# Performance work log

Hardware: AMD Instinct MI355X
Metric: run time of the kernel (lower is better)

## Reference

```python
import jax, jax.numpy as jnp
import numpy as np

NH = 16  # num_heads


def _ln(x, eps=1e-6):
    m = x.mean(-1, keepdims=True)
    v = ((x - m) ** 2).mean(-1, keepdims=True)
    return (x - m) * jax.lax.rsqrt(v + eps)


def _mod(z, sh, sc):
    return z * (1 + sc[:, None, :]) + sh[:, None, :]


def _attn(q, k, v, out_w, out_b, nh=NH):
    B, S, E = q.shape
    hd = E // nh
    q = q.reshape(B, S, nh, hd)
    k = k.reshape(B, -1, nh, hd)
    v = v.reshape(B, -1, nh, hd)
    s = jnp.einsum('bqhd,bkhd->bhqk', q, k) / float(np.sqrt(hd))
    a = jax.nn.softmax(s, axis=-1)
    o = jnp.einsum('bhqk,bkhd->bqhd', a, v).reshape(B, S, E)
    return o @ out_w.T + out_b


def setup_inputs() -> dict:
    key = jax.random.key(0)
    ks = jax.random.split(key, 40)
    E, L, Ne, I, p, C, clip, Kd = 1024, 2, 8, 4096, 2, 4, 768, 1536
    N = (64 // p) ** 2
    n = lambda k, shape, s=0.02: (jax.random.normal(k, shape, jnp.float32) * s)
    inp = {
        'x': jax.random.normal(ks[0], (2, C, 64, 64), jnp.float32),
        't': jax.random.uniform(ks[1], (2,), jnp.float32) * 1000.0,
        'clip_vec': jax.random.normal(ks[2], (2, clip), jnp.float32),
        'qwen_context': jax.random.normal(ks[3], (2, 256, Kd), jnp.float32),
        'conv_w': n(ks[4], (E, C, p, p)),
        'conv_b': n(ks[5], (E,)),
        'pos_embed': n(ks[6], (1, N, E)),
        'tmlp_w1': n(ks[7], (256, 256)), 'tmlp_b1': n(ks[8], (256,)),
        'tmlp_w2': n(ks[9], (256, 256)), 'tmlp_b2': n(ks[10], (256,)),
        'cond_w': n(ks[11], (E, 256 + clip)), 'cond_b': n(ks[12], (E,)),
        'ada_w': n(ks[13], (L, 9 * E, E)), 'ada_b': n(ks[14], (L, 9 * E)),
        'sa_in_w': n(ks[15], (L, 3 * E, E)), 'sa_in_b': n(ks[16], (L, 3 * E)),
        'sa_out_w': n(ks[17], (L, E, E)), 'sa_out_b': n(ks[18], (L, E)),
        'ca_q_w': n(ks[19], (L, E, E)), 'ca_k_w': n(ks[20], (L, E, Kd)),
        'ca_v_w': n(ks[21], (L, E, Kd)), 'ca_in_b': n(ks[22], (L, 3 * E)),
        'ca_out_w': n(ks[23], (L, E, E)), 'ca_out_b': n(ks[24], (L, E)),
        'gate_w': n(ks[25], (L, Ne, E)), 'gate_b': n(ks[26], (L, Ne)),
        'e_w1': n(ks[27], (L, Ne, I, E)), 'e_b1': n(ks[28], (L, Ne, I)),
        'e_w2': n(ks[29], (L, Ne, E, I)), 'e_b2': n(ks[30], (L, Ne, E)),
        'fin_w': n(ks[31], (p * p * C, E)), 'fin_b': n(ks[32], (p * p * C,)),
    }
    return inp


def reference(x, t, clip_vec, qwen_context, conv_w, conv_b, pos_embed,
              tmlp_w1, tmlp_b1, tmlp_w2, tmlp_b2, cond_w, cond_b,
              ada_w, ada_b, sa_in_w, sa_in_b, sa_out_w, sa_out_b,
              ca_q_w, ca_k_w, ca_v_w, ca_in_b, ca_out_w, ca_out_b,
              gate_w, gate_b, e_w1, e_b1, e_w2, e_b2, fin_w, fin_b):
    B, C, H, W = x.shape
    E, p = conv_w.shape[0], conv_w.shape[-1]
    h, w = H // p, W // p
    # patch-embed conv (kernel==stride) as unfold + matmul
    patches = x.reshape(B, C, h, p, w, p).transpose(0, 2, 4, 1, 3, 5).reshape(B, h * w, C * p * p)
    xt = patches @ conv_w.reshape(E, -1).T + conv_b + pos_embed
    # sinusoidal timestep embedding (dim 256)
    half = 128
    freqs = jnp.exp(jnp.arange(half, dtype=jnp.float32) * (-np.log(10000.0) / (half - 1)))
    te = t[:, None] * freqs[None, :]
    te = jnp.concatenate([jnp.sin(te), jnp.cos(te)], -1)
    te = jax.nn.silu(te @ tmlp_w1.T + tmlp_b1) @ tmlp_w2.T + tmlp_b2
    c = jnp.concatenate([te, clip_vec], -1) @ cond_w.T + cond_b  # [B,E]
    depth = ada_w.shape[0]
    for i in range(depth):
        pr = jax.nn.silu(c) @ ada_w[i].T + ada_b[i]
        sh_sa, sc_sa, g_sa, sh_ca, sc_ca, g_ca, sh_m, sc_m, g_m = jnp.split(pr, 9, axis=1)
        # self-attention
        xn = _mod(_ln(xt), sh_sa, sc_sa)
        qkv = xn @ sa_in_w[i].T + sa_in_b[i]
        q, k, v = jnp.split(qkv, 3, axis=-1)
        xt = xt + g_sa[:, None, :] * _attn(q, k, v, sa_out_w[i], sa_out_b[i])
        # cross-attention with separate q/k/v projections
        xn = _mod(_ln(xt), sh_ca, sc_ca)
        q = xn @ ca_q_w[i].T + ca_in_b[i, :E]
        k = qwen_context @ ca_k_w[i].T + ca_in_b[i, E:2 * E]
        v = qwen_context @ ca_v_w[i].T + ca_in_b[i, 2 * E:]
        xt = xt + g_ca[:, None, :] * _attn(q, k, v, ca_out_w[i], ca_out_b[i])
        # top-2 sparse MoE (dense-combine formulation: zero weight for unrouted experts)
        xn = _mod(_ln(xt), sh_m, sc_m)
        probs = jax.nn.softmax(xn @ gate_w[i].T + gate_b[i], axis=-1)
        tw, ti = jax.lax.top_k(probs, 2)
        tw = tw / (tw.sum(-1, keepdims=True) + 1e-6)
        wd = (jax.nn.one_hot(ti, probs.shape[-1], dtype=xn.dtype) * tw[..., None]).sum(-2)  # [B,S,Ne]
        hid = jax.nn.gelu(jnp.einsum('bsd,eid->bsei', xn, e_w1[i]) + e_b1[i], approximate=True)
        y = jnp.einsum('bsei,eoi->bseo', hid, e_w2[i]) + e_b2[i]
        moe = jnp.einsum('bseo,bse->bso', y, wd)
        xt = xt + g_m[:, None, :] * moe
    # final layer + unpatchify (nhwpqc->nchpwq)
    xt = _ln(xt) @ fin_w.T + fin_b
    out = xt.reshape(B, h, w, p, p, C).transpose(0, 5, 1, 3, 2, 4).reshape(B, C, h * p, w * p)
    return out
```

## Files before the change

kernel.cpp:

```cpp
#include <hip/hip_runtime.h>
#include <hip/hip_bf16.h>

#define B_ 2
#define S_ 1024
#define E_ 1024
#define NHEAD 16
#define NE 8
#define II 4096
#define KD 1536
#define CLIP_ 768
#define TOK (B_*S_)
#define NSLOTP 5120

typedef short bf16x8 __attribute__((ext_vector_type(8)));
typedef float f32x4 __attribute__((ext_vector_type(4)));

__device__ __forceinline__ float siluf(float x){ return x/(1.f+expf(-x)); }
__device__ __forceinline__ float geluf(float x){
    float x3 = x*x*x;
    return 0.5f*x*(1.f+tanhf(0.7978845608028654f*(x+0.044715f*x3)));
}
__device__ __forceinline__ unsigned short h16(float x){
    union { __hip_bfloat16 b; unsigned short u; } c;
    c.b = __float2bfloat16(x);
    return c.u;
}
__device__ __forceinline__ unsigned pk2(float a, float b){
    return (unsigned)h16(a) | ((unsigned)h16(b)<<16);
}
__device__ __forceinline__ void sp(float a, unsigned& hb, unsigned& lb){
    unsigned short h = h16(a);
    float r = a - __uint_as_float(((unsigned)h)<<16);
    hb = h; lb = h16(r);
}
__device__ __forceinline__ size_t pidx(int row, int k, int K){
    return (((size_t)(row>>4)*(K>>5) + (k>>5))<<9) + (((k>>3)&3)<<7) + ((row&15)<<3) + (k&7);
}

union U8 { unsigned u[4]; bf16x8 v; uint4 q; };

__global__ void k_patch_embed(const float* __restrict__ x, const float* __restrict__ cw,
                              const float* __restrict__ cb, const float* __restrict__ pos,
                              float* __restrict__ xt){
    int token = blockIdx.x;
    int b = token >> 10, n = token & 1023;
    int hh = n >> 5, ww = n & 31;
    __shared__ float patch[16];
    int tid = threadIdx.x;
    if (tid < 16){
        int c = tid >> 2, py = (tid >> 1) & 1, px = tid & 1;
        patch[tid] = x[(((size_t)b*4 + c)*64 + hh*2+py)*64 + ww*2+px];
    }
    __syncthreads();
    for (int e = tid; e < E_; e += 256){
        float acc = cb[e];
        #pragma unroll
        for (int j=0;j<16;j++) acc += patch[j]*cw[e*16+j];
        xt[(size_t)token*E_ + e] = acc + pos[(size_t)n*E_ + e];
    }
}

__global__ void k_time_cond(const float* __restrict__ t, const float* __restrict__ clip,
                            const float* __restrict__ w1, const float* __restrict__ b1,
                            const float* __restrict__ w2, const float* __restrict__ b2,
                            const float* __restrict__ cw, const float* __restrict__ cbias,
                            float* __restrict__ silu_c){
    int b = blockIdx.x, tid = threadIdx.x;
    __shared__ float te[256], h1[256], te2[256];
    if (tid < 128){
        float f = expf((float)tid * (-9.210340371976184f/127.f));
        float a = t[b]*f;
        te[tid]     = sinf(a);
        te[tid+128] = cosf(a);
    }
    __syncthreads();
    {
        float acc = b1[tid];
        const float* wr = w1 + (size_t)tid*256;
        for (int k=0;k<256;k++) acc += te[k]*wr[k];
        h1[tid] = siluf(acc);
    }
    __syncthreads();
    {
        float acc = b2[tid];
        const float* wr = w2 + (size_t)tid*256;
        for (int k=0;k<256;k++) acc += h1[k]*wr[k];
        te2[tid] = acc;
    }
    __syncthreads();
    const float* cl = clip + (size_t)b*CLIP_;
    for (int e = tid; e < E_; e += 256){
        float acc = cbias[e];
        const float* wr = cw + (size_t)e*1024;
        for (int k=0;k<256;k++)  acc += te2[k]*wr[k];
        for (int k=0;k<CLIP_;k++) acc += cl[k]*wr[256+k];
        silu_c[b*E_+e] = siluf(acc);
    }
}

__global__ void k_ada2(const float* __restrict__ sic, const float* __restrict__ aw,
                       const float* __restrict__ ab, float* __restrict__ pr){
    int row = blockIdx.x*4 + (threadIdx.x>>6);
    int lane = threadIdx.x & 63;
    const float* w = aw + (size_t)row*1024;
    float a0 = 0.f, a1 = 0.f;
    #pragma unroll
    for (int it=0; it<4; it++){
        int k = it*256 + lane*4;
        float4 wv = *(const float4*)(w+k);
        float4 x0 = *(const float4*)(sic+k);
        float4 x1 = *(const float4*)(sic+1024+k);
        a0 += wv.x*x0.x + wv.y*x0.y + wv.z*x0.z + wv.w*x0.w;
        a1 += wv.x*x1.x + wv.y*x1.y + wv.z*x1.z + wv.w*x1.w;
    }
    #pragma unroll
    for (int off=32; off; off>>=1){ a0 += __shfl_down(a0,off); a1 += __shfl_down(a1,off); }
    if (lane==0){
        float bb = ab[row];
        pr[row] = a0 + bb;
        pr[9*E_ + row] = a1 + bb;
    }
}

template<int PACK>
__global__ void k_ln_mod(const float* __restrict__ src, float* __restrict__ dst32,
                         unsigned short* __restrict__ dsth, unsigned short* __restrict__ dstl,
                         const float* __restrict__ pr, int shc, int scc){
    int token = blockIdx.x, tid = threadIdx.x;
    int b = token >> 10;
    const float* row = src + (size_t)token*E_;
    float4 v = *(const float4*)(row + tid*4);
    float s = v.x+v.y+v.z+v.w;
    float ss = v.x*v.x+v.y*v.y+v.z*v.z+v.w*v.w;
    #pragma unroll
    for (int off=32; off; off>>=1){ s += __shfl_down(s,off); ss += __shfl_down(ss,off); }
    __shared__ float rs_[4], rss_[4];
    int wid = tid >> 6;
    if ((tid&63)==0){ rs_[wid]=s; rss_[wid]=ss; }
    __syncthreads();
    s  = rs_[0]+rs_[1]+rs_[2]+rs_[3];
    ss = rss_[0]+rss_[1]+rss_[2]+rss_[3];
    float mean = s*(1.f/1024.f);
    float rstd = rsqrtf(ss*(1.f/1024.f) - mean*mean + 1e-6f);
    const float* shv = pr + b*9*E_ + shc*E_;
    const float* scv = pr + b*9*E_ + scc*E_;
    int e = tid*4;
    float o[4];
    float4 sc4 = *(const float4*)(scv+e);
    float4 sh4 = *(const float4*)(shv+e);
    o[0] = (v.x-mean)*rstd*(1.f+sc4.x) + sh4.x;
    o[1] = (v.y-mean)*rstd*(1.f+sc4.y) + sh4.y;
    o[2] = (v.z-mean)*rstd*(1.f+sc4.z) + sh4.z;
    o[3] = (v.w-mean)*rstd*(1.f+sc4.w) + sh4.w;
    unsigned hu[2], lu[2];
    {
        unsigned h0,l0,h1,l1;
        sp(o[0],h0,l0); sp(o[1],h1,l1);
        hu[0]=h0|(h1<<16); lu[0]=l0|(l1<<16);
        sp(o[2],h0,l0); sp(o[3],h1,l1);
        hu[1]=h0|(h1<<16); lu[1]=l0|(l1<<16);
    }
    if (PACK){
        size_t base = pidx(token, e, E_);
        *(uint2*)(dsth + base) = make_uint2(hu[0],hu[1]);
        *(uint2*)(dstl + base) = make_uint2(lu[0],lu[1]);
    } else {
        *(float4*)(dst32 + (size_t)token*E_ + e) = make_float4(o[0],o[1],o[2],o[3]);
        *(uint2*)(dsth + (size_t)token*E_ + e) = make_uint2(hu[0],hu[1]);
        *(uint2*)(dstl + (size_t)token*E_ + e) = make_uint2(lu[0],lu[1]);
    }
}

__global__ void k_pack_qwen(const float* __restrict__ q, unsigned short* __restrict__ hp,
                            unsigned short* __restrict__ lp){
    int r = blockIdx.x;
    int k = threadIdx.x*8;
    float f[8];
    *(float4*)(f+0) = *(const float4*)(q + (size_t)r*KD + k);
    *(float4*)(f+4) = *(const float4*)(q + (size_t)r*KD + k + 4);
    U8 H, L;
    #pragma unroll
    for (int i=0;i<4;i++){
        unsigned h0,l0,h1,l1;
        sp(f[2*i],h0,l0); sp(f[2*i+1],h1,l1);
        H.u[i] = h0|(h1<<16); L.u[i] = l0|(l1<<16);
    }
    size_t dst = pidx(r, k, KD);
    *(uint4*)(hp + dst) = H.q;
    *(uint4*)(lp + dst) = L.q;
}

__global__ void k_gather_pack(const unsigned short* __restrict__ xh,
                              const unsigned short* __restrict__ xl,
                              const int* __restrict__ list,
                              unsigned short* __restrict__ oh, unsigned short* __restrict__ ol){
    int s = blockIdx.x;
    int tid = threadIdx.x;
    int token = list[s];
    int k = tid*8;
    size_t src = (size_t)token*E_ + k;
    size_t dst = pidx(s, k, E_);
    *(uint4*)(oh + dst) = *(const uint4*)(xh + src);
    *(uint4*)(ol + dst) = *(const uint4*)(xl + src);
}

template<int MOE, int EPI, int TERMS, int SPLITK=1>
__global__ __launch_bounds__(256) void k_mm(
    const unsigned short* __restrict__ Ah, const unsigned short* __restrict__ Al,
    const float* __restrict__ Wp, int ldw,
    const float* __restrict__ biasp, int bstride,
    void* __restrict__ Cp, void* __restrict__ Cp2, int ldc,
    int M, int N, int K,
    const float* __restrict__ pr, int gch,
    const int* __restrict__ cnt, const int* __restrict__ offs)
{
    constexpr int NPL = (TERMS==3) ? 2 : 1;
    int e  = MOE ? blockIdx.z : 0;
    int Mm = MOE ? cnt[e] : M;
    int bm = blockIdx.y*128;
    if (MOE && bm >= Mm) return;
    int o0 = MOE ? offs[e] : 0;
    int nt = gridDim.x / SPLITK;
    int ntile = blockIdx.x % nt;
    int kc = blockIdx.x / nt;
    int bn = ntile*128;
    int kbeg = kc*(K/SPLITK), kend = kbeg + K/SPLITK;
    const float* W = Wp + (size_t)e*N*ldw;
    const float* bias = biasp + (size_t)e*bstride;

    __shared__ __align__(16) unsigned short Bs_[2][NPL][128*40];

    int tid = threadIdx.x;
    int lane = tid & 63, wid = tid >> 6;
    int wm = wid >> 1, wn = wid & 1;
    int fr = lane & 15, fko = (lane>>4)*8, fr4 = (lane>>4)*4;
    int lane8 = lane<<3;
    int K32 = K>>5;

    int rgm[4];
    #pragma unroll
    for (int m=0;m<4;m++) rgm[m] = ((MOE?o0:0) + bm + wm*64 + m*16) >> 4;

    auto LA = [&](int m, int k0, bf16x8& h, bf16x8& l){
        size_t off = (((size_t)rgm[m]*K32 + (k0>>5))<<9) + lane8;
        h = *(const bf16x8*)(Ah + off);
        if (TERMS==3) l = *(const bf16x8*)(Al + off);
    };

    int srow = tid >> 1, shalf = tid & 1;
    int sbase = srow*40 + shalf*16;
    const float* Bf = W + (size_t)(bn + srow)*ldw + shalf*16;

    float fB[16];
    auto LOADB = [&](int k0){
        *(float4*)(fB+0)  = *(const float4*)(Bf+k0+0);
        *(float4*)(fB+4)  = *(const float4*)(Bf+k0+4);
        *(float4*)(fB+8)  = *(const float4*)(Bf+k0+8);
        *(float4*)(fB+12) = *(const float4*)(Bf+k0+12);
    };
    auto STAGEB = [&](int buf){
        if (TERMS==3){
            unsigned hb2[8], lb2[8];
            #pragma unroll
            for (int i=0;i<8;i++){
                unsigned h0,l0,h1,l1;
                sp(fB[2*i],h0,l0); sp(fB[2*i+1],h1,l1);
                hb2[i]=h0|(h1<<16); lb2[i]=l0|(l1<<16);
            }
            *(uint4*)&Bs_[buf][0][sbase]   = make_uint4(hb2[0],hb2[1],hb2[2],hb2[3]);
            *(uint4*)&Bs_[buf][0][sbase+8] = make_uint4(hb2[4],hb2[5],hb2[6],hb2[7]);
            *(uint4*)&Bs_[buf][NPL-1][sbase]   = make_uint4(lb2[0],lb2[1],lb2[2],lb2[3]);
            *(uint4*)&Bs_[buf][NPL-1][sbase+8] = make_uint4(lb2[4],lb2[5],lb2[6],lb2[7]);
        } else {
            unsigned hb2[8];
            #pragma unroll
            for (int i=0;i<8;i++) hb2[i] = pk2(fB[2*i],fB[2*i+1]);
            *(uint4*)&Bs_[buf][0][sbase]   = make_uint4(hb2[0],hb2[1],hb2[2],hb2[3]);
            *(uint4*)&Bs_[buf][0][sbase+8] = make_uint4(hb2[4],hb2[5],hb2[6],hb2[7]);
        }
    };

    f32x4 acc[4][4];
    #pragma unroll
    for (int m=0;m<4;m++)
        #pragma unroll
        for (int n=0;n<4;n++) acc[m][n] = (f32x4){0.f,0.f,0.f,0.f};

    bf16x8 ah[4], al[4];
    #pragma unroll
    for (int m=0;m<4;m++) LA(m, kbeg, ah[m], al[m]);
    LOADB(kbeg);
    STAGEB(0);
    __syncthreads();
    int cur = 0;
    for (int k0=kbeg; k0<kend; k0+=32){
        bool nxt = (k0+32) < kend;
        if (nxt) LOADB(k0+32);
        bf16x8 bh[4], bl[4];
        #pragma unroll
        for (int n=0;n<4;n++){
            int off = (wn*64 + n*16 + fr)*40 + fko;
            bh[n] = *(const bf16x8*)&Bs_[cur][0][off];
            if (TERMS==3) bl[n] = *(const bf16x8*)&Bs_[cur][NPL-1][off];
        }
        #pragma unroll
        for (int m=0;m<4;m++){
            #pragma unroll
            for (int n=0;n<4;n++){
                acc[m][n] = __builtin_amdgcn_mfma_f32_16x16x32_bf16(ah[m], bh[n], acc[m][n], 0, 0, 0);
                if (TERMS==3){
                    acc[m][n] = __builtin_amdgcn_mfma_f32_16x16x32_bf16(ah[m], bl[n], acc[m][n], 0, 0, 0);
                    acc[m][n] = __builtin_amdgcn_mfma_f32_16x16x32_bf16(al[m], bh[n], acc[m][n], 0, 0, 0);
                }
            }
            if (nxt) LA(m, k0+32, ah[m], al[m]);
        }
        if (nxt) STAGEB(cur^1);
        __syncthreads();
        cur ^= 1;
    }

    #pragma unroll
    for (int m=0;m<4;m++){
        #pragma unroll
        for (int j=0;j<4;j++){
            int row = bm + wm*64 + m*16 + fr4 + j;
            if (EPI != 2 && row >= Mm) continue;
            #pragma unroll
            for (int n=0;n<4;n++){
                int col = bn + wn*64 + n*16 + fr;
                float bv = (SPLITK==1 || kc==0) ? bias[col] : 0.f;
                float v = acc[m][n][j] + bv;
                if (EPI==0){
                    ((float*)Cp)[(size_t)row*ldc + col] = v;
                } else if (EPI==1){
                    int bb = row >> 10;
                    ((float*)Cp)[(size_t)row*ldc + col] += pr[bb*9*E_ + gch*E_ + col] * v;
                } else if (EPI==2){
                    int prow = o0 + row;
                    size_t pi = pidx(prow, col, II);
                    if (TERMS==3){
                        unsigned hb, lb; sp(geluf(v), hb, lb);
                        ((unsigned short*)Cp )[pi] = (unsigned short)hb;
                        ((unsigned short*)Cp2)[pi] = (unsigned short)lb;
                    } else {
                        ((unsigned short*)Cp )[pi] = h16(geluf(v));
                    }
                } else {
                    if (SPLITK==1)
                        ((float*)Cp)[(size_t)(o0+row)*ldc + col] = v;
                    else
                        atomicAdd(&((float*)Cp)[(size_t)(o0+row)*ldc + col], v);
                }
            }
        }
    }
}

__global__ __launch_bounds__(256) void k_attn_m(
    const float* __restrict__ qp, int qstride,
    const float* __restrict__ kp, const float* __restrict__ vp, int kvstride,
    unsigned short* __restrict__ oph, unsigned short* __restrict__ opl,
    int Sq, int Sk, float scale)
{
    __shared__ __align__(16) unsigned short Kh[64*72];
    __shared__ __align__(16) unsigned short Kl[64*72];
    __shared__ __align__(16) unsigned V_i[64*70];
    __shared__ __align__(16) unsigned short P_[4][2][16*72];

    int tid = threadIdx.x, lane = tid & 63, wid = tid >> 6;
    int g = lane >> 4, fr = lane & 15;
    int h = blockIdx.y, b = blockIdx.z;
    int qbase = blockIdx.x*64;

    bf16x8 qh[2], ql[2];
    {
        const float* qr = qp + (size_t)(b*Sq + qbase + wid*16 + fr)*qstride + h*64;
        #pragma unroll
        for (int ds=0; ds<2; ds++){
            float f[8];
            *(float4*)(f+0) = *(const float4*)(qr + ds*32 + g*8);
            *(float4*)(f+4) = *(const float4*)(qr + ds*32 + g*8 + 4);
            U8 uh, ul;
            #pragma unroll
            for (int i=0;i<4;i++){
                unsigned h0,l0,h1,l1;
                sp(f[2*i]*scale, h0,l0); sp(f[2*i+1]*scale, h1,l1);
                uh.u[i] = h0|(h1<<16); ul.u[i] = l0|(l1<<16);
            }
            qh[ds] = uh.v; ql[ds] = ul.v;
        }
    }

    float m_run = -1e30f, l_run = 0.f;
    f32x4 oacc[4];
    #pragma unroll
    for (int dt=0;dt<4;dt++) oacc[dt] = (f32x4){0.f,0.f,0.f,0.f};

    unsigned short* PhW = &P_[wid][0][0];
    unsigned short* PlW = &P_[wid][1][0];

    for (int kt0 = 0; kt0 < Sk; kt0 += 64){
        __syncthreads();
        {
            int srow = tid >> 2, d0 = (tid & 3) << 4;
            size_t grow = (size_t)(b*Sk + kt0 + srow)*kvstride + h*64 + d0;
            {
                const float* srcp = kp + grow;
                float f[16];
                *(float4*)(f+0)  = *(const float4*)(srcp+0);
                *(float4*)(f+4)  = *(const float4*)(srcp+4);
                *(float4*)(f+8)  = *(const float4*)(srcp+8);
                *(float4*)(f+12) = *(const float4*)(srcp+12);
                U8 uh0, uh1, ul0, ul1;
                #pragma unroll
                for (int i=0;i<4;i++){
                    unsigned a0,b0,a1,b1;
                    sp(f[2*i],a0,b0); sp(f[2*i+1],a1,b1);
                    uh0.u[i] = a0|(a1<<16); ul0.u[i] = b0|(b1<<16);
                }
                #pragma unroll
                for (int i=0;i<4;i++){
                    unsigned a0,b0,a1,b1;
                    sp(f[8+2*i],a0,b0); sp(f[8+2*i+1],a1,b1);
                    uh1.u[i] = a0|(a1<<16); ul1.u[i] = b0|(b1<<16);
                }
                int base = srow*72 + d0;
                *(uint4*)&Kh[base]     = uh0.q;
                *(uint4*)&Kh[base + 8] = uh1.q;
                *(uint4*)&Kl[base]     = ul0.q;
                *(uint4*)&Kl[base + 8] = ul1.q;
            }
            {
                const float* srcp = vp + grow;
                float f[16];
                *(float4*)(f+0)  = *(const float4*)(srcp+0);
                *(float4*)(f+4)  = *(const float4*)(srcp+4);
                *(float4*)(f+8)  = *(const float4*)(srcp+8);
                *(float4*)(f+12) = *(const float4*)(srcp+12);
                int base = srow*70 + d0;
                #pragma unroll
                for (int i4=0;i4<4;i4++){
                    U8 u;
                    #pragma unroll
                    for (int i=0;i<4;i++){
                        unsigned hb, lb; sp(f[4*i4+i], hb, lb);
                        u.u[i] = hb | (lb<<16);
                    }
                    *(uint2*)&V_i[base + i4*4]     = make_uint2(u.u[0], u.u[1]);
                    *(uint2*)&V_i[base + i4*4 + 2] = make_uint2(u.u[2], u.u[3]);
                }
            }
        }
        __syncthreads();

        f32x4 st[4];
        #pragma unroll
        for (int kt=0;kt<4;kt++) st[kt] = (f32x4){0.f,0.f,0.f,0.f};
        #pragma unroll
        for (int ds=0; ds<2; ds++){
            #pragma unroll
            for (int kt=0;kt<4;kt++){
                int row = kt*16 + fr;
                int so = row*72 + ds*32 + g*8;
                bf16x8 kh  = *(const bf16x8*)&Kh[so];
                bf16x8 klo = *(const bf16x8*)&Kl[so];
                st[kt] = __builtin_amdgcn_mfma_f32_16x16x32_bf16(kh, qh[ds], st[kt], 0,0,0);
                st[kt] = __builtin_amdgcn_mfma_f32_16x16x32_bf16(kh, ql[ds], st[kt], 0,0,0);
                st[kt] = __builtin_amdgcn_mfma_f32_16x16x32_bf16(klo, qh[ds], st[kt], 0,0,0);
            }
        }

        float pmax = -1e30f;
        #pragma unroll
        for (int kt=0;kt<4;kt++)
            #pragma unroll
            for (int r=0;r<4;r++) pmax = fmaxf(pmax, st[kt][r]);
        pmax = fmaxf(pmax, __shfl_xor(pmax, 16));
        pmax = fmaxf(pmax, __shfl_xor(pmax, 32));
        float mnew = fmaxf(m_run, pmax);
        float p[4][4]; float psum = 0.f;
        #pragma unroll
        for (int kt=0;kt<4;kt++)
            #pragma unroll
            for (int r=0;r<4;r++){ float pv = expf(st[kt][r] - mnew); p[kt][r] = pv; psum += pv; }
        psum += __shfl_xor(psum, 16);
        psum += __shfl_xor(psum, 32);
        float corr = expf(m_run - mnew);
        l_run = l_run*corr + psum;
        m_run = mnew;
        #pragma unroll
        for (int j=0;j<4;j++){
            float cj = __shfl(corr, g*4 + j);
            #pragma unroll
            for (int dt=0;dt<4;dt++) oacc[dt][j] *= cj;
        }

        #pragma unroll
        for (int kt=0;kt<4;kt++){
            unsigned h0,l0,h1,l1,h2,l2,h3,l3;
            sp(p[kt][0],h0,l0); sp(p[kt][1],h1,l1);
            sp(p[kt][2],h2,l2); sp(p[kt][3],h3,l3);
            int base = fr*72 + kt*16 + g*4;
            *(unsigned*)&PhW[base]     = h0|(h1<<16);
            *(unsigned*)&PhW[base + 2] = h2|(h3<<16);
            *(unsigned*)&PlW[base]     = l0|(l1<<16);
            *(unsigned*)&PlW[base + 2] = l2|(l3<<16);
        }

        #pragma unroll
        for (int ks=0; ks<2; ks++){
            int pso = fr*72 + ks*32 + g*8;
            bf16x8 ph = *(const bf16x8*)&PhW[pso];
            bf16x8 pl = *(const bf16x8*)&PlW[pso];
            #pragma unroll
            for (int dt=0; dt<4; dt++){
                unsigned w[8];
                #pragma unroll
                for (int j=0;j<8;j++){
                    int row = ks*32 + g*8 + j;
                    w[j] = V_i[row*70 + dt*16 + fr];
                }
                U8 vh, vl;
                #pragma unroll
                for (int i=0;i<4;i++){
                    vh.u[i] = (w[2*i] & 0xffffu) | (w[2*i+1] << 16);
                    vl.u[i] = (w[2*i] >> 16)     | (w[2*i+1] & 0xffff0000u);
                }
                oacc[dt] = __builtin_amdgcn_mfma_f32_16x16x32_bf16(ph, vh.v, oacc[dt], 0,0,0);
                oacc[dt] = __builtin_amdgcn_mfma_f32_16x16x32_bf16(ph, vl.v, oacc[dt], 0,0,0);
                oacc[dt] = __builtin_amdgcn_mfma_f32_16x16x32_bf16(pl, vh.v, oacc[dt], 0,0,0);
            }
        }
    }

    float linv = 1.f / l_run;
    #pragma unroll
    for (int j=0;j<4;j++){
        float lj = __shfl(linv, g*4 + j);
        int row = b*Sq + qbase + wid*16 + g*4 + j;
        #pragma unroll
        for (int dt=0;dt<4;dt++){
            unsigned hb, lb; sp(oacc[dt][j]*lj, hb, lb);
            int k = h*64 + dt*16 + fr;
            size_t pi = pidx(row, k, E_);
            oph[pi] = (unsigned short)hb;
            opl[pi] = (unsigned short)lb;
        }
    }
}

__global__ void k_route(const float* __restrict__ xn, const float* __restrict__ gw,
                        const float* __restrict__ gb, int* __restrict__ i01,
                        float* __restrict__ w01, int* __restrict__ cnt){
    int token = blockIdx.x, lane = threadIdx.x;
    const float* row = xn + (size_t)token*E_;
    float part[8] = {0,0,0,0,0,0,0,0};
    for (int k = lane; k < E_; k += 64){
        float xv = row[k];
        #pragma unroll
        for (int e=0;e<8;e++) part[e] += xv*gw[e*E_+k];
    }
    #pragma unroll
    for (int e=0;e<8;e++){
        #pragma unroll
        for (int off=32; off; off>>=1) part[e] += __shfl_down(part[e], off);
    }
    if (lane==0){
        float lg[8]; float mx = -1e30f;
        #pragma unroll
        for (int e=0;e<8;e++){ lg[e] = part[e]+gb[e]; if (lg[e]>mx) mx = lg[e]; }
        float sum = 0.f;
        #pragma unroll
        for (int e=0;e<8;e++){ lg[e] = expf(lg[e]-mx); sum += lg[e]; }
        int a0 = 0;
        #pragma unroll
        for (int e=1;e<8;e++) if (lg[e] > lg[a0]) a0 = e;
        int a1 = (a0==0)?1:0;
        #pragma unroll
        for (int e=0;e<8;e++) if (e!=a0 && lg[e] > lg[a1]) a1 = e;
        float p0 = lg[a0]/sum, p1 = lg[a1]/sum;
        float inv = 1.f/(p0+p1+1e-6f);
        i01[token*2+0]=a0; i01[token*2+1]=a1;
        w01[token*2+0]=p0*inv; w01[token*2+1]=p1*inv;
        atomicAdd(&cnt[a0],1); atomicAdd(&cnt[a1],1);
    }
}

__global__ void k_scan(const int* __restrict__ cnt, int* __restrict__ offs, int* __restrict__ curs){
    if (threadIdx.x==0 && blockIdx.x==0){
        int o = 0;
        for (int e=0;e<8;e++){
            offs[e]=o; curs[e]=o;
            o += ((cnt[e]+127)>>7)<<7;
        }
    }
}

__global__ void k_place(const int* __restrict__ i01,
                        int* __restrict__ curs, int* __restrict__ list,
                        int* __restrict__ t2s){
    int t = blockIdx.x*256 + threadIdx.x;
    if (t >= TOK) return;
    #pragma unroll
    for (int s=0;s<2;s++){
        int e = i01[t*2+s];
        int p = atomicAdd(&curs[e],1);
        list[p] = t;
        t2s[t*2+s] = p;
    }
}

__global__ void k_moe_combine2(float* __restrict__ xt, const float* __restrict__ yslot,
                               const int* __restrict__ t2s, const float* __restrict__ w01,
                               const float* __restrict__ pr){
    int idx = blockIdx.x*256 + threadIdx.x;
    int token = idx >> 10, n = idx & 1023;
    int b = token >> 10;
    int s0 = t2s[token*2], s1 = t2s[token*2+1];
    float mo = w01[token*2]*yslot[(size_t)s0*E_+n] + w01[token*2+1]*yslot[(size_t)s1*E_+n];
    xt[idx] += pr[b*9*E_ + 8*E_ + n]*mo;
}

__global__ void k_final(const float* __restrict__ xt, const float* __restrict__ fw,
                        const float* __restrict__ fb, float* __restrict__ out){
    int token = blockIdx.x, tid = threadIdx.x;
    int b = token >> 10, n = token & 1023, hh = n >> 5, ww = n & 31;
    const float* row = xt + (size_t)token*E_;
    float4 v = *(const float4*)(row + tid*4);
    float s = v.x+v.y+v.z+v.w;
    float ss = v.x*v.x+v.y*v.y+v.z*v.z+v.w*v.w;
    #pragma unroll
    for (int off=32; off; off>>=1){ s += __shfl_down(s,off); ss += __shfl_down(ss,off); }
    __shared__ float rs_[4], rss_[4];
    int wid = tid >> 6;
    if ((tid&63)==0){ rs_[wid]=s; rss_[wid]=ss; }
    __syncthreads();
    s  = rs_[0]+rs_[1]+rs_[2]+rs_[3];
    ss = rss_[0]+rss_[1]+rss_[2]+rss_[3];
    float mean = s*(1.f/1024.f);
    float rstd = rsqrtf(ss*(1.f/1024.f) - mean*mean + 1e-6f);
    __shared__ float xl[1024];
    int e = tid*4;
    xl[e+0]=(v.x-mean)*rstd; xl[e+1]=(v.y-mean)*rstd;
    xl[e+2]=(v.z-mean)*rstd; xl[e+3]=(v.w-mean)*rstd;
    __syncthreads();
    int o = tid & 15, seg = tid >> 4;
    float part = 0.f;
    const float* wr = fw + (size_t)o*E_ + seg*64;
    const float* xr = xl + seg*64;
    #pragma unroll 8
    for (int j=0;j<64;j++) part += xr[j]*wr[j];
    __shared__ float ps[16][17];
    ps[seg][o] = part;
    __syncthreads();
    if (tid < 16){
        float acc = fb[tid];
        #pragma unroll
        for (int s2=0;s2<16;s2++) acc += ps[s2][tid];
        int py = tid>>3, px = (tid>>2)&1, ch = tid&3;
        out[(((size_t)b*4+ch)*64 + hh*2+py)*64 + ww*2+px] = acc;
    }
}

extern "C" void kernel_launch(void* const* d_in, const int* in_sizes, int n_in,
                              void* d_out, int out_size, void* d_ws, size_t ws_size,
                              hipStream_t stream){
    const float* x        = (const float*)d_in[0];
    const float* t        = (const float*)d_in[1];
    const float* clip     = (const float*)d_in[2];
    const float* qwen     = (const float*)d_in[3];
    const float* conv_w   = (const float*)d_in[4];
    const float* conv_b   = (const float*)d_in[5];
    const float* pos      = (const float*)d_in[6];
    const float* tw1      = (const float*)d_in[7];
    const float* tb1      = (const float*)d_in[8];
    const float* tw2      = (const float*)d_in[9];
    const float* tb2      = (const float*)d_in[10];
    const float* cond_w   = (const float*)d_in[11];
    const float* cond_b   = (const float*)d_in[12];
    const float* ada_w    = (const float*)d_in[13];
    const float* ada_b    = (const float*)d_in[14];
    const float* sa_in_w  = (const float*)d_in[15];
    const float* sa_in_b  = (const float*)d_in[16];
    const float* sa_out_w = (const float*)d_in[17];
    const float* sa_out_b = (const float*)d_in[18];
    const float* ca_q_w   = (const float*)d_in[19];
    const float* ca_k_w   = (const float*)d_in[20];
    const float* ca_v_w   = (const float*)d_in[21];
    const float* ca_in_b  = (const float*)d_in[22];
    const float* ca_out_w = (const float*)d_in[23];
    const float* ca_out_b = (const float*)d_in[24];
    const float* gate_w   = (const float*)d_in[25];
    const float* gate_b   = (const float*)d_in[26];
    const float* e_w1     = (const float*)d_in[27];
    const float* e_b1     = (const float*)d_in[28];
    const float* e_w2     = (const float*)d_in[29];
    const float* e_b2     = (const float*)d_in[30];
    const float* fin_w    = (const float*)d_in[31];
    const float* fin_b    = (const float*)d_in[32];

    float* ws    = (float*)d_ws;
    float* xt    = ws;
    float* xn    = ws + 2097152;
    float* qkv   = ws + 4194304;
    float* yslot = qkv;
    unsigned short* xnh  = (unsigned short*)(ws + 10485760);
    unsigned short* xnl  = (unsigned short*)(ws + 11534336);
    unsigned short* obh  = (unsigned short*)(ws + 12582912);
    unsigned short* obl  = (unsigned short*)(ws + 13631488);
    unsigned short* xnsh = (unsigned short*)(ws + 14680064);
    unsigned short* xnsl = (unsigned short*)(ws + 17301504);
    unsigned short* hidh = (unsigned short*)(ws + 19922944);
    unsigned short* hidl = (unsigned short*)(ws + 30408704);
    unsigned short* qwph = (unsigned short*)(ws + 40894464);
    unsigned short* qwpl = (unsigned short*)(ws + 41287680);
    float* kbuf  = ws + 41680896;
    float* vbuf  = ws + 42205184;
    float* pr    = ws + 42729472;
    float* sic   = ws + 42747904;
    float* w01   = ws + 42749952;
    int*   i01   = (int*)(ws + 42754048);
    int*   t2s   = (int*)(ws + 42758144);
    int*   list  = (int*)(ws + 42762240);
    int*   cnt   = (int*)(ws + 42767360);
    int*   offs  = cnt + 8;
    int*   curs  = cnt + 16;

    k_patch_embed<<<TOK,256,0,stream>>>(x, conv_w, conv_b, pos, xt);
    k_time_cond<<<B_,256,0,stream>>>(t, clip, tw1, tb1, tw2, tb2, cond_w, cond_b, sic);
    k_pack_qwen<<<B_*256,192,0,stream>>>(qwen, qwph, qwpl);

    for (int i=0;i<2;i++){
        k_ada2<<<2304,256,0,stream>>>(sic, ada_w + (size_t)i*9*E_*E_,
                                      ada_b + (size_t)i*9*E_, pr);
        k_ln_mod<1><<<TOK,256,0,stream>>>(xt, nullptr, xnh, xnl, pr, 0, 1);
        k_mm<0,0,3><<<dim3(24,16),256,0,stream>>>(
            xnh, xnl, sa_in_w + (size_t)i*3*E_*E_, E_, sa_in_b + (size_t)i*3*E_, 0,
            qkv, nullptr, 3*E_, TOK, 3*E_, E_, nullptr, 0, nullptr, nullptr);
        k_attn_m<<<dim3(16,NHEAD,B_),256,0,stream>>>(qkv, 3*E_, qkv+E_, qkv+2*E_, 3*E_,
                                                     obh, obl, S_, S_, 0.125f);
        k_mm<0,1,3><<<dim3(8,16),256,0,stream>>>(
            obh, obl, sa_out_w + (size_t)i*E_*E_, E_, sa_out_b + (size_t)i*E_, 0,
            xt, nullptr, E_, TOK, E_, E_, pr, 2, nullptr, nullptr);
        k_ln_mod<1><<<TOK,256,0,stream>>>(xt, nullptr, xnh, xnl, pr, 3, 4);
        k_mm<0,0,3><<<dim3(8,16),256,0,stream>>>(
            xnh, xnl, ca_q_w + (size_t)i*E_*E_, E_, ca_in_b + (size_t)i*3*E_, 0,
            qkv, nullptr, E_, TOK, E_, E_, nullptr, 0, nullptr, nullptr);
        k_mm<0,0,3><<<dim3(8,4),256,0,stream>>>(
            qwph, qwpl, ca_k_w + (size_t)i*E_*KD, KD, ca_in_b + (size_t)i*3*E_ + E_, 0,
            kbuf, nullptr, E_, B_*256, E_, KD, nullptr, 0, nullptr, nullptr);
        k_mm<0,0,3><<<dim3(8,4),256,0,stream>>>(
            qwph, qwpl, ca_v_w + (size_t)i*E_*KD, KD, ca_in_b + (size_t)i*3*E_ + 2*E_, 0,
            vbuf, nullptr, E_, B_*256, E_, KD, nullptr, 0, nullptr, nullptr);
        k_attn_m<<<dim3(16,NHEAD,B_),256,0,stream>>>(qkv, E_, kbuf, vbuf, E_,
                                                     obh, obl, S_, 256, 0.125f);
        k_mm<0,1,3><<<dim3(8,16),256,0,stream>>>(
            obh, obl, ca_out_w + (size_t)i*E_*E_, E_, ca_out_b + (size_t)i*E_, 0,
            xt, nullptr, E_, TOK, E_, E_, pr, 5, nullptr, nullptr);
        k_ln_mod<0><<<TOK,256,0,stream>>>(xt, xn, xnh, xnl, pr, 6, 7);
        hipMemsetAsync(cnt, 0, 8*sizeof(int), stream);
        hipMemsetAsync(list, 0, NSLOTP*sizeof(int), stream);
        k_route<<<TOK,64,0,stream>>>(xn, gate_w + (size_t)i*NE*E_, gate_b + (size_t)i*NE,
                                     i01, w01, cnt);
        k_scan<<<1,64,0,stream>>>(cnt, offs, curs);
        k_place<<<TOK/256,256,0,stream>>>(i01, curs, list, t2s);
        k_gather_pack<<<NSLOTP,128,0,stream>>>(xnh, xnl, list, xnsh, xnsl);
        hipMemsetAsync(yslot, 0, (size_t)NSLOTP*E_*sizeof(float), stream);
        if (i==0){
            k_mm<1,2,3><<<dim3(32,32,NE),256,0,stream>>>(
                xnsh, xnsl, e_w1 + (size_t)i*NE*II*E_, E_, e_b1 + (size_t)i*NE*II, II,
                hidh, hidl, II, 0, II, E_, nullptr, 0, cnt, offs);
            k_mm<1,3,3,4><<<dim3(32,32,NE),256,0,stream>>>(
                hidh, hidl, e_w2 + (size_t)i*NE*E_*II, II, e_b2 + (size_t)i*NE*E_, E_,
                yslot, nullptr, E_, 0, E_, II, nullptr, 0, cnt, offs);
        } else {
            k_mm<1,2,1><<<dim3(32,32,NE),256,0,stream>>>(
                xnsh, nullptr, e_w1 + (size_t)i*NE*II*E_, E_, e_b1 + (size_t)i*NE*II, II,
                hidh, nullptr, II, 0, II, E_, nullptr, 0, cnt, offs);
            k_mm<1,3,1,4><<<dim3(32,32,NE),256,0,stream>>>(
                hidh, nullptr, e_w2 + (size_t)i*NE*E_*II, II, e_b2 + (size_t)i*NE*E_, E_,
                yslot, nullptr, E_, 0, E_, II, nullptr, 0, cnt, offs);
        }
        k_moe_combine2<<<TOK*E_/256,256,0,stream>>>(xt, yslot, t2s, w01, pr);
    }
    k_final<<<TOK,256,0,stream>>>(xt, fin_w, fin_b, (float*)d_out);
}
```

Baseline: 2.325 ms.

## Pre-pack weights into bf16 hi/lo MFMA tiles and stream via global_load_lds

Adds a weight-packing kernel that splits fp32 weights into bf16 hi/lo planes in the MFMA tile layout before each GEMM. The GEMM kernel then loads both A and B tiles directly into LDS with global_load_lds and double-buffers them, which removes the per-block fp32-to-bf16 split of B that was repeated for every M tile. Expert weights are packed four experts at a time into a shared scratch buffer. The cost is extra packing kernels and extra memory traffic, because the weights are read in fp32 and written back as bf16 on every call. The LDS tile layout may also cause bank conflicts.

```diff
diff --git a/kernel.cpp b/kernel.cpp
--- a/kernel.cpp
+++ b/kernel.cpp
@@ -35,6 +35,10 @@
 }
 __device__ __forceinline__ size_t pidx(int row, int k, int K){
     return (((size_t)(row>>4)*(K>>5) + (k>>5))<<9) + (((k>>3)&3)<<7) + ((row&15)<<3) + (k&7);
+}
+__device__ __forceinline__ void gload16(const unsigned short* g, unsigned short* l){
+    __builtin_amdgcn_global_load_lds((const __attribute__((address_space(1))) void*)g,
+                                     (__attribute__((address_space(3))) void*)l, 16, 0, 0);
 }
 
 union U8 { unsigned u[4]; bf16x8 v; uint4 q; };
@@ -204,17 +208,46 @@
     *(uint4*)(ol + dst) = *(const uint4*)(xl + src);
 }
 
+template<int NPL>
+__global__ void k_pack_w(const float* __restrict__ W, unsigned short* __restrict__ hp,
+                         unsigned short* __restrict__ lp, int K){
+    int rg = blockIdx.x;
+    int t = threadIdx.x;
+    int K32 = K>>5;
+    for (int k = t*8; k < K; k += 1024){
+        size_t bb = (((size_t)rg*K32 + (k>>5))<<9) + (((k>>3)&3)<<7);
+        #pragma unroll 4
+        for (int r=0;r<16;r++){
+            const float* src = W + (size_t)(rg*16 + r)*K + k;
+            float f[8];
+            *(float4*)(f)   = *(const float4*)src;
+            *(float4*)(f+4) = *(const float4*)(src+4);
+            U8 H, L;
+            #pragma unroll
+            for (int i2=0;i2<4;i2++){
+                unsigned h0,l0,h1,l1;
+                sp(f[2*i2],h0,l0); sp(f[2*i2+1],h1,l1);
+                H.u[i2]=h0|(h1<<16); L.u[i2]=l0|(l1<<16);
+            }
+            *(uint4*)(hp + bb + (r<<3)) = H.q;
+            if (NPL==2) *(uint4*)(lp + bb + (r<<3)) = L.q;
+        }
+    }
+}
+
 template<int MOE, int EPI, int TERMS, int SPLITK=1>
 __global__ __launch_bounds__(256) void k_mm(
     const unsigned short* __restrict__ Ah, const unsigned short* __restrict__ Al,
-    const float* __restrict__ Wp, int ldw,
+    const unsigned short* __restrict__ Bh, const unsigned short* __restrict__ Bl,
     const float* __restrict__ biasp, int bstride,
     void* __restrict__ Cp, void* __restrict__ Cp2, int ldc,
     int M, int N, int K,
     const float* __restrict__ pr, int gch,
     const int* __restrict__ cnt, const int* __restrict__ offs)
 {
-    constexpr int NPL = (TERMS==3) ? 2 : 1;
+    constexpr int NPL = (TERMS==3)?2:1;
+    constexpr int NB  = 2*NPL*8;
+    constexpr int NBW = NB/4;
     int e  = MOE ? blockIdx.z : 0;
     int Mm = MOE ? cnt[e] : M;
     int bm = blockIdx.y*128;
@@ -222,63 +255,35 @@
     int o0 = MOE ? offs[e] : 0;
     int nt = gridDim.x / SPLITK;
     int ntile = blockIdx.x % nt;
-    int kc = blockIdx.x / nt;
+    int kc0 = blockIdx.x / nt;
     int bn = ntile*128;
-    int kbeg = kc*(K/SPLITK), kend = kbeg + K/SPLITK;
-    const float* W = Wp + (size_t)e*N*ldw;
+    int K32 = K >> 5;
+    int kbeg = kc0*(K/SPLITK), kend = kbeg + K/SPLITK;
     const float* bias = biasp + (size_t)e*bstride;
 
-    __shared__ __align__(16) unsigned short Bs_[2][NPL][128*40];
-
-    int tid = threadIdx.x;
-    int lane = tid & 63, wid = tid >> 6;
-    int wm = wid >> 1, wn = wid & 1;
-    int fr = lane & 15, fko = (lane>>4)*8, fr4 = (lane>>4)*4;
-    int lane8 = lane<<3;
-    int K32 = K>>5;
-
-    int rgm[4];
-    #pragma unroll
-    for (int m=0;m<4;m++) rgm[m] = ((MOE?o0:0) + bm + wm*64 + m*16) >> 4;
-
-    auto LA = [&](int m, int k0, bf16x8& h, bf16x8& l){
-        size_t off = (((size_t)rgm[m]*K32 + (k0>>5))<<9) + lane8;
-        h = *(const bf16x8*)(Ah + off);
-        if (TERMS==3) l = *(const bf16x8*)(Al + off);
-    };
-
-    int srow = tid >> 1, shalf = tid & 1;
-    int sbase = srow*40 + shalf*16;
-    const float* Bf = W + (size_t)(bn + srow)*ldw + shalf*16;
-
-    float fB[16];
-    auto LOADB = [&](int k0){
-        *(float4*)(fB+0)  = *(const float4*)(Bf+k0+0);
-        *(float4*)(fB+4)  = *(const float4*)(Bf+k0+4);
-        *(float4*)(fB+8)  = *(const float4*)(Bf+k0+8);
-        *(float4*)(fB+12) = *(const float4*)(Bf+k0+12);
-    };
-    auto STAGEB = [&](int buf){
-        if (TERMS==3){
-            unsigned hb2[8], lb2[8];
-            #pragma unroll
-            for (int i=0;i<8;i++){
-                unsigned h0,l0,h1,l1;
-                sp(fB[2*i],h0,l0); sp(fB[2*i+1],h1,l1);
-                hb2[i]=h0|(h1<<16); lb2[i]=l0|(l1<<16);
-            }
-            *(uint4*)&Bs_[buf][0][sbase]   = make_uint4(hb2[0],hb2[1],hb2[2],hb2[3]);
-            *(uint4*)&Bs_[buf][0][sbase+8] = make_uint4(hb2[4],hb2[5],hb2[6],hb2[7]);
-            *(uint4*)&Bs_[buf][NPL-1][sbase]   = make_uint4(lb2[0],lb2[1],lb2[2],lb2[3]);
-            *(uint4*)&Bs_[buf][NPL-1][sbase+8] = make_uint4(lb2[4],lb2[5],lb2[6],lb2[7]);
-        } else {
-            unsigned hb2[8];
-            #pragma unroll
-            for (int i=0;i<8;i++) hb2[i] = pk2(fB[2*i],fB[2*i+1]);
-            *(uint4*)&Bs_[buf][0][sbase]   = make_uint4(hb2[0],hb2[1],hb2[2],hb2[3]);
-            *(uint4*)&Bs_[buf][0][sbase+8] = make_uint4(hb2[4],hb2[5],hb2[6],hb2[7]);
-        }
-    };
+    __shared__ __align__(16) unsigned short LDm[2][NB*512];
+
+    int tid = threadIdx.x, lane = tid&63, wid = tid>>6;
+    int wm = wid>>1, wn = wid&1;
+    int fr = lane&15, fr4 = (lane>>4)*4;
+    int l8 = lane<<3;
+    int a16 = ((MOE? o0:0) + bm) >> 4;
+    int b16 = bn >> 4;
+    size_t eoff = (size_t)e * N * K;
+
+    const unsigned short* gb[NBW];
+    #pragma unroll
+    for (int i=0;i<NBW;i++){
+        int bidx = wid*NBW + i;
+        int isB = (bidx >= NPL*8) ? 1 : 0;
+        int r = bidx - isB*NPL*8;
+        int pl = r>>3, rg = r&7;
+        const unsigned short* p;
+        size_t rgg;
+        if (!isB){ p = (TERMS==3 && pl)? Al : Ah; rgg = (size_t)(a16 + rg); }
+        else     { p = ((TERMS==3 && pl)? Bl : Bh) + eoff; rgg = (size_t)(b16 + rg); }
+        gb[i] = p + ((rgg*K32)<<9) + l8;
+    }
 
     f32x4 acc[4][4];
     #pragma unroll
@@ -286,25 +291,35 @@
         #pragma unroll
         for (int n=0;n<4;n++) acc[m][n] = (f32x4){0.f,0.f,0.f,0.f};
 
-    bf16x8 ah[4], al[4];
-    #pragma unroll
-    for (int m=0;m<4;m++) LA(m, kbeg, ah[m], al[m]);
-    LOADB(kbeg);
-    STAGEB(0);
+    {
+        int kc = kbeg>>5;
+        #pragma unroll
+        for (int i=0;i<NBW;i++)
+            gload16(gb[i] + ((size_t)kc<<9), &LDm[0][(size_t)(wid*NBW+i)<<9]);
+    }
     __syncthreads();
     int cur = 0;
     for (int k0=kbeg; k0<kend; k0+=32){
         bool nxt = (k0+32) < kend;
-        if (nxt) LOADB(k0+32);
-        bf16x8 bh[4], bl[4];
+        if (nxt){
+            int kc = (k0+32)>>5;
+            #pragma unroll
+            for (int i=0;i<NBW;i++)
+                gload16(gb[i] + ((size_t)kc<<9), &LDm[cur^1][(size_t)(wid*NBW+i)<<9]);
+        }
+        bf16x8 ah[4], al[4], bh[4], bl[4];
+        #pragma unroll
+        for (int m=0;m<4;m++){
+            ah[m] = *(const bf16x8*)&LDm[cur][(size_t)((wm*4+m)<<9) + l8];
+            if (TERMS==3) al[m] = *(const bf16x8*)&LDm[cur][(size_t)((8+wm*4+m)<<9) + l8];
+        }
         #pragma unroll
         for (int n=0;n<4;n++){
-            int off = (wn*64 + n*16 + fr)*40 + fko;
-            bh[n] = *(const bf16x8*)&Bs_[cur][0][off];
-            if (TERMS==3) bl[n] = *(const bf16x8*)&Bs_[cur][NPL-1][off];
-        }
-        #pragma unroll
-        for (int m=0;m<4;m++){
+            bh[n] = *(const bf16x8*)&LDm[cur][(size_t)((NPL*8 + wn*4+n)<<9) + l8];
+            if (TERMS==3) bl[n] = *(const bf16x8*)&LDm[cur][(size_t)((NPL*8+8 + wn*4+n)<<9) + l8];
+        }
+        #pragma unroll
+        for (int m=0;m<4;m++)
             #pragma unroll
             for (int n=0;n<4;n++){
                 acc[m][n] = __builtin_amdgcn_mfma_f32_16x16x32_bf16(ah[m], bh[n], acc[m][n], 0, 0, 0);
@@ -313,9 +328,6 @@
                     acc[m][n] = __builtin_amdgcn_mfma_f32_16x16x32_bf16(al[m], bh[n], acc[m][n], 0, 0, 0);
                 }
             }
-            if (nxt) LA(m, k0+32, ah[m], al[m]);
-        }
-        if (nxt) STAGEB(cur^1);
         __syncthreads();
         cur ^= 1;
     }
@@ -329,7 +341,7 @@
             #pragma unroll
             for (int n=0;n<4;n++){
                 int col = bn + wn*64 + n*16 + fr;
-                float bv = (SPLITK==1 || kc==0) ? bias[col] : 0.f;
+                float bv = (SPLITK==1 || kc0==0) ? bias[col] : 0.f;
                 float v = acc[m][n][j] + bv;
                 if (EPI==0){
                     ((float*)Cp)[(size_t)row*ldc + col] = v;
@@ -337,8 +349,7 @@
                     int bb = row >> 10;
                     ((float*)Cp)[(size_t)row*ldc + col] += pr[bb*9*E_ + gch*E_ + col] * v;
                 } else if (EPI==2){
-                    int prow = o0 + row;
-                    size_t pi = pidx(prow, col, II);
+                    size_t pi = pidx(o0 + row, col, II);
                     if (TERMS==3){
                         unsigned hb, lb; sp(geluf(v), hb, lb);
                         ((unsigned short*)Cp )[pi] = (unsigned short)hb;
@@ -726,6 +737,12 @@
     int*   cnt   = (int*)(ws + 42767360);
     int*   offs  = cnt + 8;
     int*   curs  = cnt + 16;
+    unsigned short* wb = (unsigned short*)(ws + 42768384);
+
+    const size_t SA_IN_H=0, SA_IN_L=3145728, SA_OUT_H=6291456, SA_OUT_L=7340032;
+    const size_t CAQ_H=8388608, CAQ_L=9437184, CAK_H=10485760, CAK_L=12058624;
+    const size_t CAV_H=13631488, CAV_L=15204352, CAO_H=16777216, CAO_L=17825792;
+    const size_t W_H=0, W_L=16777216;
 
     k_patch_embed<<<TOK,256,0,stream>>>(x, conv_w, conv_b, pos, xt);
     k_time_cond<<<B_,256,0,stream>>>(t, clip, tw1, tb1, tw2, tb2, cond_w, cond_b, sic);
@@ -734,29 +751,35 @@
     for (int i=0;i<2;i++){
         k_ada2<<<2304,256,0,stream>>>(sic, ada_w + (size_t)i*9*E_*E_,
                                       ada_b + (size_t)i*9*E_, pr);
+        k_pack_w<2><<<192,128,0,stream>>>(sa_in_w + (size_t)i*3*E_*E_, wb+SA_IN_H, wb+SA_IN_L, E_);
+        k_pack_w<2><<<64,128,0,stream>>>(sa_out_w + (size_t)i*E_*E_, wb+SA_OUT_H, wb+SA_OUT_L, E_);
+        k_pack_w<2><<<64,128,0,stream>>>(ca_q_w + (size_t)i*E_*E_, wb+CAQ_H, wb+CAQ_L, E_);
+        k_pack_w<2><<<64,128,0,stream>>>(ca_k_w + (size_t)i*E_*KD, wb+CAK_H, wb+CAK_L, KD);
+        k_pack_w<2><<<64,128,0,stream>>>(ca_v_w + (size_t)i*E_*KD, wb+CAV_H, wb+CAV_L, KD);
+        k_pack_w<2><<<64,128,0,stream>>>(ca_out_w + (size_t)i*E_*E_, wb+CAO_H, wb+CAO_L, E_);
         k_ln_mod<1><<<TOK,256,0,stream>>>(xt, nullptr, xnh, xnl, pr, 0, 1);
         k_mm<0,0,3><<<dim3(24,16),256,0,stream>>>(
-            xnh, xnl, sa_in_w + (size_t)i*3*E_*E_, E_, sa_in_b + (size_t)i*3*E_, 0,
+            xnh, xnl, wb+SA_IN_H, wb+SA_IN_L, sa_in_b + (size_t)i*3*E_, 0,
             qkv, nullptr, 3*E_, TOK, 3*E_, E_, nullptr, 0, nullptr, nullptr);
         k_attn_m<<<dim3(16,NHEAD,B_),256,0,stream>>>(qkv, 3*E_, qkv+E_, qkv+2*E_, 3*E_,
                                                      obh, obl, S_, S_, 0.125f);
         k_mm<0,1,3><<<dim3(8,16),256,0,stream>>>(
-            obh, obl, sa_out_w + (size_t)i*E_*E_, E_, sa_out_b + (size_t)i*E_, 0,
+            obh, obl, wb+SA_OUT_H, wb+SA_OUT_L, sa_out_b + (size_t)i*E_, 0,
             xt, nullptr, E_, TOK, E_, E_, pr, 2, nullptr, nullptr);
         k_ln_mod<1><<<TOK,256,0,stream>>>(xt, nullptr, xnh, xnl, pr, 3, 4);
         k_mm<0,0,3><<<dim3(8,16),256,0,stream>>>(
-            xnh, xnl, ca_q_w + (size_t)i*E_*E_, E_, ca_in_b + (size_t)i*3*E_, 0,
+            xnh, xnl, wb+CAQ_H, wb+CAQ_L, ca_in_b + (size_t)i*3*E_, 0,
             qkv, nullptr, E_, TOK, E_, E_, nullptr, 0, nullptr, nullptr);
         k_mm<0,0,3><<<dim3(8,4),256,0,stream>>>(
-            qwph, qwpl, ca_k_w + (size_t)i*E_*KD, KD, ca_in_b + (size_t)i*3*E_ + E_, 0,
+            qwph, qwpl, wb+CAK_H, wb+CAK_L, ca_in_b + (size_t)i*3*E_ + E_, 0,
             kbuf, nullptr, E_, B_*256, E_, KD, nullptr, 0, nullptr, nullptr);
         k_mm<0,0,3><<<dim3(8,4),256,0,stream>>>(
-            qwph, qwpl, ca_v_w + (size_t)i*E_*KD, KD, ca_in_b + (size_t)i*3*E_ + 2*E_, 0,
+            qwph, qwpl, wb+CAV_H, wb+CAV_L, ca_in_b + (size_t)i*3*E_ + 2*E_, 0,
             vbuf, nullptr, E_, B_*256, E_, KD, nullptr, 0, nullptr, nullptr);
         k_attn_m<<<dim3(16,NHEAD,B_),256,0,stream>>>(qkv, E_, kbuf, vbuf, E_,
                                                      obh, obl, S_, 256, 0.125f);
         k_mm<0,1,3><<<dim3(8,16),256,0,stream>>>(
-            obh, obl, ca_out_w + (size_t)i*E_*E_, E_, ca_out_b + (size_t)i*E_, 0,
+            obh, obl, wb+CAO_H, wb+CAO_L, ca_out_b + (size_t)i*E_, 0,
             xt, nullptr, E_, TOK, E_, E_, pr, 5, nullptr, nullptr);
         k_ln_mod<0><<<TOK,256,0,stream>>>(xt, xn, xnh, xnl, pr, 6, 7);
         hipMemsetAsync(cnt, 0, 8*sizeof(int), stream);
@@ -767,20 +790,31 @@
         k_place<<<TOK/256,256,0,stream>>>(i01, curs, list, t2s);
         k_gather_pack<<<NSLOTP,128,0,stream>>>(xnh, xnl, list, xnsh, xnsl);
         hipMemsetAsync(yslot, 0, (size_t)NSLOTP*E_*sizeof(float), stream);
-        if (i==0){
-            k_mm<1,2,3><<<dim3(32,32,NE),256,0,stream>>>(
-                xnsh, xnsl, e_w1 + (size_t)i*NE*II*E_, E_, e_b1 + (size_t)i*NE*II, II,
-                hidh, hidl, II, 0, II, E_, nullptr, 0, cnt, offs);
-            k_mm<1,3,3,4><<<dim3(32,32,NE),256,0,stream>>>(
-                hidh, hidl, e_w2 + (size_t)i*NE*E_*II, II, e_b2 + (size_t)i*NE*E_, E_,
-                yslot, nullptr, E_, 0, E_, II, nullptr, 0, cnt, offs);
-        } else {
-            k_mm<1,2,1><<<dim3(32,32,NE),256,0,stream>>>(
-                xnsh, nullptr, e_w1 + (size_t)i*NE*II*E_, E_, e_b1 + (size_t)i*NE*II, II,
-                hidh, nullptr, II, 0, II, E_, nullptr, 0, cnt, offs);
-            k_mm<1,3,1,4><<<dim3(32,32,NE),256,0,stream>>>(
-                hidh, nullptr, e_w2 + (size_t)i*NE*E_*II, II, e_b2 + (size_t)i*NE*E_, E_,
-                yslot, nullptr, E_, 0, E_, II, nullptr, 0, cnt, offs);
+        for (int e0=0;e0<NE;e0+=4){
+            if (i==0){
+                k_pack_w<2><<<1024,128,0,stream>>>(e_w1 + ((size_t)i*NE+e0)*II*E_, wb+W_H, wb+W_L, E_);
+                k_mm<1,2,3><<<dim3(32,32,4),256,0,stream>>>(
+                    xnsh, xnsl, wb+W_H, wb+W_L, e_b1 + (size_t)i*NE*II + (size_t)e0*II, II,
+                    hidh, hidl, II, 0, II, E_, nullptr, 0, cnt+e0, offs+e0);
+            } else {
+                k_pack_w<1><<<1024,128,0,stream>>>(e_w1 + ((size_t)i*NE+e0)*II*E_, wb+W_H, nullptr, E_);
+                k_mm<1,2,1><<<dim3(32,32,4),256,0,stream>>>(
+                    xnsh, nullptr, wb+W_H, nullptr, e_b1 + (size_t)i*NE*II + (size_t)e0*II, II,
+                    hidh, nullptr, II, 0, II, E_, nullptr, 0, cnt+e0, offs+e0);
+            }
+        }
+        for (int e0=0;e0<NE;e0+=4){
+            if (i==0){
+                k_pack_w<2><<<256,128,0,stream>>>(e_w2 + ((size_t)i*NE+e0)*E_*II, wb+W_H, wb+W_L, II);
+                k_mm<1,3,3,4><<<dim3(32,32,4),256,0,stream>>>(
+                    hidh, hidl, wb+W_H, wb+W_L, e_b2 + (size_t)i*NE*E_ + (size_t)e0*E_, E_,
+                    yslot, nullptr, E_, 0, E_, II, nullptr, 0, cnt+e0, offs+e0);
+            } else {
+                k_pack_w<1><<<256,128,0,stream>>>(e_w2 + ((size_t)i*NE+e0)*E_*II, wb+W_H, nullptr, II);
+                k_mm<1,3,1,4><<<dim3(32,32,4),256,0,stream>>>(
+                    hidh, nullptr, wb+W_H, nullptr, e_b2 + (size_t)i*NE*E_ + (size_t)e0*E_, E_,
+                    yslot, nullptr, E_, 0, E_, II, nullptr, 0, cnt+e0, offs+e0);
+            }
         }
         k_moe_combine2<<<TOK*E_/256,256,0,stream>>>(xt, yslot, t2s, w01, pr);
     }
```

Measured after the change: 2.407 ms. +3.5%, slower.
